# Kernel optimization log

Hardware: AMD Instinct MI355X
Metric: run time of the kernel (lower is better)

## Reference

```python
import jax, jax.numpy as jnp
import numpy as np

BATCH = 128
SITES = 256      # input_dim, number of MPS input cores
BOND = 64        # bond dimension D
FEAT = 2         # feature_dim
OUT = 10         # output_dim


def setup_inputs() -> dict:
    key = jax.random.key(0)
    k1, k2, k3, k4, k5 = jax.random.split(key, 5)
    # forward input: [batch, input_dim, feature_dim], values in [0,1) like a feature map
    input_data = jax.random.uniform(k1, (BATCH, SITES, FEAT), dtype=jnp.float32)
    # InputRegion core tensor, bond_str 'slri' -> [sites, D, D, feat]
    # small random perturbation; identity bias (use_bias=True, fixed_bias) added in forward
    cores = 0.01 * jax.random.normal(k2, (SITES, BOND, BOND, FEAT), dtype=jnp.float32)
    # OutputSite core, bond_str 'olr' -> [output_dim, D, D]
    out_core = 0.01 * jax.random.normal(k3, (OUT, BOND, BOND), dtype=jnp.float32)
    # boundary (edge) vectors for open boundary conditions
    left_vec = jax.random.normal(k4, (BOND,), dtype=jnp.float32) / np.sqrt(BOND)
    right_vec = jax.random.normal(k5, (BOND,), dtype=jnp.float32) / np.sqrt(BOND)
    return {"input_data": input_data, "cores": cores, "out_core": out_core,
            "left_vec": left_vec, "right_vec": right_vec}


def _chain_matmul(mats):
    """Log-depth product of a chain of matrices. mats: [b, s, D, D] -> [b, D, D].
    Product is ordered: mats[:,0] @ mats[:,1] @ ... @ mats[:,s-1]."""
    b, s, d, _ = mats.shape
    while mats.shape[1] > 1:
        n = mats.shape[1]
        if n % 2 == 1:  # pad with identity so length is even
            eye = jnp.broadcast_to(jnp.eye(d, dtype=mats.dtype), (b, 1, d, d))
            mats = jnp.concatenate([mats, eye], axis=1)
        mats = jnp.matmul(mats[:, 0::2], mats[:, 1::2])
    return mats[:, 0]


def reference(input_data, cores, out_core, left_vec, right_vec):
    # InputRegion.forward: contract each core with its per-site feature vector
    # 'slri,bsi->bslr', then add identity bias matrix (use_bias=True)
    mats = jnp.einsum('slri,bsi->bslr', cores, input_data)
    mats = mats + jnp.eye(BOND, dtype=mats.dtype)  # bias_mat = eye, broadcast over b,s

    # split the chain around the (central) output site, reduce each side
    half = SITES // 2
    left_prod = _chain_matmul(mats[:, :half])    # [b, D, D]
    right_prod = _chain_matmul(mats[:, half:])   # [b, D, D]

    # open-boundary contraction: lvec . Lprod . out_core . Rprod . rvec -> [b, out]
    v = jnp.einsum('l,blr->br', left_vec, left_prod)        # [b, D]
    v = jnp.einsum('bl,olr->bor', v, out_core)              # [b, out, D]
    v = jnp.einsum('bol,blr->bor', v, right_prod)           # [b, out, D]
    logits = jnp.einsum('bor,r->bo', v, right_vec)          # [b, out]
    return logits
```

## Files before the change

### kernel.cpp

```cpp
#include <hip/hip_runtime.h>

#define BOND   64
#define SITES  256
#define HALF   128
#define NBATCH 128
#define OUTD   10

#define P1_OFF   1048576
#define VEC_OFF  2097152
#define SITE_F4  2048
#define LPITCH   132

__global__ void __launch_bounds__(256)
mps_pack_kernel(const float* __restrict__ cores, float* __restrict__ P) {
  __shared__ __align__(16) float ld[64 * LPITCH];
  const int s = (int)blockIdx.x;
  const int t = (int)threadIdx.x;
  const float4* src = (const float4*)(cores + (size_t)s * 8192);
  #pragma unroll
  for (int k = 0; k < 8; ++k) {
    const int m = t + 256 * k;
    const int row = m >> 5;
    const int c4  = m & 31;
    *(float4*)&ld[row * LPITCH + c4 * 4] = src[m];
  }
  __syncthreads();
  const bool right = s >= HALF;
  const int step = right ? (SITES - 1 - s) : s;
  float4* out = (float4*)(P + (right ? P1_OFF : 0)) + (size_t)step * SITE_F4;
  #pragma unroll
  for (int k = 0; k < 8; ++k) {
    const int m = t + 256 * k;
    const int g = m >> 6;
    const int j = m & 63;
    float4 v;
    if (!right) {
      const float2 a  = *(const float2*)&ld[(2 * g) * LPITCH + 2 * j];
      const float2 b2 = *(const float2*)&ld[(2 * g + 1) * LPITCH + 2 * j];
      v = make_float4(a.x, a.y, b2.x, b2.y);
    } else {
      v = *(const float4*)&ld[j * LPITCH + 4 * g];
    }
    out[m] = v;
  }
}

__global__ void __launch_bounds__(64, 1)
mps_chain_kernel(const float* __restrict__ input,
                 const float* __restrict__ P,
                 const float* __restrict__ lvec,
                 const float* __restrict__ rvec,
                 float* __restrict__ vout) {
  __shared__ __align__(16) float vbuf[BOND];
  __shared__ __align__(16) float xsh[HALF][2];

  const int lane = (int)threadIdx.x;
  const int side = (int)blockIdx.x & 1;
  const int b    = (int)blockIdx.x >> 1;

  {
    const float4 g =
        ((const float4*)(input + (size_t)b * SITES * 2 + side * HALF * 2))[lane];
    if (!side) {
      ((float4*)xsh)[lane] = g;
    } else {
      ((float2*)xsh)[HALF - 1 - 2 * lane] = make_float2(g.x, g.y);
      ((float2*)xsh)[HALF - 2 - 2 * lane] = make_float2(g.z, g.w);
    }
  }

  float r = side ? rvec[lane] : lvec[lane];

  const float4* base = (const float4*)(P + (side ? P1_OFF : 0)) + lane;

  float4 A[32], B[32];
  #pragma unroll
  for (int j = 0; j < 32; ++j) A[j] = base[j * 64];

  #define STEP(CUR, NXT, I)                                                  \
  {                                                                          \
    vbuf[lane] = r;                                                          \
    float4 vv[16];                                                           \
    _Pragma("unroll")                                                        \
    for (int k = 0; k < 16; ++k) vv[k] = ((const float4*)vbuf)[k];           \
    const float2 xv = *(const float2*)xsh[(I)];                              \
    const int inx = ((I) + 1 < HALF) ? (I) + 1 : (I);                        \
    _Pragma("unroll")                                                        \
    for (int j = 0; j < 32; ++j)                                             \
      NXT[j] = base[(size_t)inx * SITE_F4 + j * 64];                         \
    __builtin_amdgcn_sched_barrier(0);   \
    float p0a = 0.f, p1a = 0.f, p0b = 0.f, p1b = 0.f;                        \
    _Pragma("unroll")                                                        \
    for (int q = 0; q < 16; ++q) {                                           \
      const float4 vq = vv[q];                            \
      const float4 m0 = CUR[2 * q];                       \
      const float4 m1 = CUR[2 * q + 1];                   \
      p0a = __builtin_fmaf(vq.x, m0.x, p0a);                                 \
      p1a = __builtin_fmaf(vq.x, m0.y, p1a);                                 \
      p0b = __builtin_fmaf(vq.z, m1.x, p0b);                                 \
      p1b = __builtin_fmaf(vq.z, m1.y, p1b);                                 \
      p0a = __builtin_fmaf(vq.y, m0.z, p0a);                                 \
      p1a = __builtin_fmaf(vq.y, m0.w, p1a);                                 \
      p0b = __builtin_fmaf(vq.w, m1.z, p0b);                                 \
      p1b = __builtin_fmaf(vq.w, m1.w, p1b);                                 \
    }                                                                        \
    r = __builtin_fmaf(xv.x, p0a + p0b, __builtin_fmaf(xv.y, p1a + p1b, r)); \
  }

  for (int i = 0; i < HALF; i += 2) {
    STEP(A, B, i);
    STEP(B, A, i + 1);
  }
  #undef STEP

  vout[((size_t)side * NBATCH + b) * BOND + lane] = r;
}

__global__ void __launch_bounds__(64)
mps_combine_kernel(const float* __restrict__ oc,
                   const float* __restrict__ vecs,
                   float* __restrict__ out) {
  __shared__ float vl[BOND];
  const int lane = (int)threadIdx.x;
  const int b = (int)blockIdx.x;
  vl[lane] = vecs[b * BOND + lane];
  const float myvr = vecs[NBATCH * BOND + b * BOND + lane];
  float res[OUTD];
  #pragma unroll
  for (int o = 0; o < OUTD; ++o) {
    float acc = 0.f;
    #pragma unroll
    for (int m = 0; m < BOND; ++m)
      acc = __builtin_fmaf(vl[m], oc[((o * BOND) + m) * BOND + lane], acc);
    acc *= myvr;
    #pragma unroll
    for (int off = 32; off > 0; off >>= 1)
      acc += __shfl_xor(acc, off, 64);
    res[o] = acc;
  }
  if (lane == 0) {
    #pragma unroll
    for (int o = 0; o < OUTD; ++o) out[b * OUTD + o] = res[o];
  }
}

extern "C" void kernel_launch(void* const* d_in, const int* in_sizes, int n_in,
                              void* d_out, int out_size, void* d_ws, size_t ws_size,
                              hipStream_t stream) {
  const float* input = (const float*)d_in[0];
  const float* cores = (const float*)d_in[1];
  const float* oc    = (const float*)d_in[2];
  const float* lvec  = (const float*)d_in[3];
  const float* rvec  = (const float*)d_in[4];
  float* ws  = (float*)d_ws;
  float* out = (float*)d_out;

  hipLaunchKernelGGL(mps_pack_kernel, dim3(SITES), dim3(256), 0, stream,
                     cores, ws);
  hipLaunchKernelGGL(mps_chain_kernel, dim3(256), dim3(64), 0, stream,
                     input, ws, lvec, rvec, ws + VEC_OFF);
  hipLaunchKernelGGL(mps_combine_kernel, dim3(NBATCH), dim3(64), 0, stream,
                     oc, ws + VEC_OFF, out);
}
```

Before: 162.3 us.

## Stage MPS chain cores into LDS with async global_load_lds double buffering

The chain kernel no longer prefetches the next site's 64x64x2 core into two 32-entry float4 register arrays. It now streams each core straight into one of two 32 KB LDS buffers with global_load_lds, then reads the current buffer back from LDS inside the FMA loop. A manual s_waitcnt vmcnt(32) lets the next site's copies stay in flight while the current site is consumed. This frees a large block of VGPRs and hands the copies to the async direct-to-LDS path. In exchange it adds 32 ds_read_b128 per step on the serial dependency chain and relies on hand-counted vmcnt ordering.

```diff
diff --git a/kernel.cpp b/kernel.cpp
--- a/kernel.cpp
+++ b/kernel.cpp
@@ -10,6 +10,10 @@
 #define VEC_OFF  2097152
 #define SITE_F4  2048
 #define LPITCH   132
+
+typedef __attribute__((ext_vector_type(4))) float f32x4;
+#define AS1 __attribute__((address_space(1)))
+#define AS3 __attribute__((address_space(3)))
 
 __global__ void __launch_bounds__(256)
 mps_pack_kernel(const float* __restrict__ cores, float* __restrict__ P) {
@@ -45,12 +49,18 @@
   }
 }
 
+__device__ __forceinline__ void gload_lds16(const float* g, float* l) {
+  __builtin_amdgcn_global_load_lds((const AS1 void*)g, (AS3 void*)l, 16, 0, 0);
+}
+
 __global__ void __launch_bounds__(64, 1)
 mps_chain_kernel(const float* __restrict__ input,
                  const float* __restrict__ P,
                  const float* __restrict__ lvec,
                  const float* __restrict__ rvec,
                  float* __restrict__ vout) {
+  __shared__ __align__(16) float buf0[8192];
+  __shared__ __align__(16) float buf1[8192];
   __shared__ __align__(16) float vbuf[BOND];
   __shared__ __align__(16) float xsh[HALF][2];
 
@@ -71,30 +81,38 @@
 
   float r = side ? rvec[lane] : lvec[lane];
 
-  const float4* base = (const float4*)(P + (side ? P1_OFF : 0)) + lane;
+  const float* gl = P + (side ? P1_OFF : 0) + lane * 4;
 
-  float4 A[32], B[32];
-  #pragma unroll
-  for (int j = 0; j < 32; ++j) A[j] = base[j * 64];
+#define STAGEL(LDST, STEPI)                                                  \
+  {                                                                          \
+    const float* gs = gl + (size_t)(STEPI) * 8192;                           \
+    _Pragma("unroll")                                                        \
+    for (int k = 0; k < 32; ++k)                                             \
+      gload_lds16(gs + k * 256, (LDST) + k * 256);                           \
+  }
 
-  #define STEP(CUR, NXT, I)                                                  \
+  STAGEL(buf0, 0);
+
+#define STEPL(BC, BN, I)                                                     \
   {                                                                          \
+          \
     vbuf[lane] = r;                                                          \
-    float4 vv[16];                                                           \
+    f32x4 vv[16];                                                            \
     _Pragma("unroll")                                                        \
-    for (int k = 0; k < 16; ++k) vv[k] = ((const float4*)vbuf)[k];           \
+    for (int k = 0; k < 16; ++k) vv[k] = ((const f32x4*)vbuf)[k];            \
     const float2 xv = *(const float2*)xsh[(I)];                              \
     const int inx = ((I) + 1 < HALF) ? (I) + 1 : (I);                        \
-    _Pragma("unroll")                                                        \
-    for (int j = 0; j < 32; ++j)                                             \
-      NXT[j] = base[(size_t)inx * SITE_F4 + j * 64];                         \
-    __builtin_amdgcn_sched_barrier(0);   \
+    STAGEL(BN, inx);                                                         \
+    asm volatile("s_waitcnt vmcnt(32)" ::: "memory");     \
+    __builtin_amdgcn_sched_barrier(0);                                       \
     float p0a = 0.f, p1a = 0.f, p0b = 0.f, p1b = 0.f;                        \
     _Pragma("unroll")                                                        \
     for (int q = 0; q < 16; ++q) {                                           \
-      const float4 vq = vv[q];                            \
-      const float4 m0 = CUR[2 * q];                       \
-      const float4 m1 = CUR[2 * q + 1];                   \
+      const f32x4 vq = vv[q];                           \
+      const f32x4 m0 =                                 \
+          *(const f32x4*)&(BC)[(2 * q) * 256 + lane * 4];                    \
+      const f32x4 m1 =                               \
+          *(const f32x4*)&(BC)[(2 * q + 1) * 256 + lane * 4];                \
       p0a = __builtin_fmaf(vq.x, m0.x, p0a);                                 \
       p1a = __builtin_fmaf(vq.x, m0.y, p1a);                                 \
       p0b = __builtin_fmaf(vq.z, m1.x, p0b);                                 \
@@ -108,10 +126,11 @@
   }
 
   for (int i = 0; i < HALF; i += 2) {
-    STEP(A, B, i);
-    STEP(B, A, i + 1);
+    STEPL(buf0, buf1, i);
+    STEPL(buf1, buf0, i + 1);
   }
-  #undef STEP
+#undef STEPL
+#undef STAGEL
 
   vout[((size_t)side * NBATCH + b) * BOND + lane] = r;
 }
```

Result: slower. 203.9 us (+25.6%).
